# Optimization experiments

Measured on AMD Instinct MI355X. Metric: run time of the kernel, lower is better.

The kernel has to match this reference:

```python
import jax, jax.numpy as jnp
import numpy as np
import math

B, S, D, H = 16, 1024, 512, 8
DPH = D // H


def _lorentz_linear(x, W, b, log_scale):
    # LorentzLinear.forward: linear map then project onto hyperboloid
    x = x @ W.T + b
    time = jax.nn.sigmoid(x[..., :1]) * jnp.exp(log_scale) + 1.0 + 1e-4
    rest = x[..., 1:]
    sq = jnp.clip(jnp.sum(rest * rest, axis=-1, keepdims=True), 1e-8, None)
    scale = (time * time - 1.0) / sq
    return jnp.concatenate([time, rest * jnp.sqrt(scale)], axis=-1)


def setup_inputs() -> dict:
    key = jax.random.key(0)
    ks = jax.random.split(key, 16)
    stdv = 1.0 / math.sqrt(D)

    def mk_w(k):
        W = jax.random.uniform(k, (D, D), minval=-stdv, maxval=stdv, dtype=jnp.float32)
        return W.at[:, 0].set(0.0)  # reset_parameters zeroes column 0

    inp = {
        'key': jax.random.normal(ks[0], (B, S, D), dtype=jnp.float32),
        'value': jax.random.normal(ks[1], (B, S, D), dtype=jnp.float32),
        'query': jax.random.normal(ks[2], (B, S, D), dtype=jnp.float32),
        'Wq': mk_w(ks[3]), 'bq': jnp.zeros((D,), jnp.float32), 'lsq': jnp.asarray(math.log(10.0), jnp.float32),
        'Wk': mk_w(ks[4]), 'bk': jnp.zeros((D,), jnp.float32), 'lsk': jnp.asarray(math.log(10.0), jnp.float32),
        'Wv': mk_w(ks[5]), 'bv': jnp.zeros((D,), jnp.float32), 'lsv': jnp.asarray(math.log(10.0), jnp.float32),
        'attn_scale': jnp.asarray([math.sqrt(D)], jnp.float32),
        'attn_bias': jnp.zeros((), jnp.float32),
    }
    return inp


def reference(key, value, query, Wq, bq, lsq, Wk, bk, lsk, Wv, bv, lsv, attn_scale, attn_bias):
    q = _lorentz_linear(query, Wq, bq, lsq)  # [B,S,D]
    k = _lorentz_linear(key, Wk, bk, lsk)
    v = _lorentz_linear(value, Wv, bv, lsv)

    def shape(x):
        b, s, _ = x.shape
        return x.reshape(b, s, H, DPH).transpose(0, 2, 1, 3)  # [B,H,S,dph]

    q, k, v = shape(q), shape(k), shape(v)

    # Minkowski signature (-,+,...,+) on the per-head feature dim
    sgn = jnp.concatenate([-jnp.ones((1,), q.dtype), jnp.ones((DPH - 1,), q.dtype)])

    # attn = (2 + 2 * cinner(q, k)) / scale + bias  (no softmax, per source)
    attn = (2.0 + 2.0 * jnp.einsum('bhqd,bhkd->bhqk', q * sgn, k)) / attn_scale + attn_bias

    # mid_point: ave = attn @ v, then normalize by sqrt(|<ave,ave>_L|)
    ave = jnp.einsum('bhqk,bhkd->bhqd', attn, v)
    inner = jnp.sum(ave * ave * sgn, axis=-1, keepdims=True)  # Lorentz inner product
    denom = jnp.sqrt(jnp.clip(jnp.abs(inner), 1e-8, None))
    ctx = ave / denom  # [B,H,S,dph]

    b = ctx.shape[0]
    return ctx.transpose(0, 2, 1, 3).reshape(b, -1, H * DPH)  # [B,S,D]
```

## Files before the change

kernel.cpp:

```cpp
#include <hip/hip_runtime.h>
#include <stdint.h>

#define B_    16
#define S_    1024
#define D_    512
#define H_    8
#define DPH_  64
#define MTOT  (B_*S_)

typedef __attribute__((ext_vector_type(8))) short  short8;
typedef __attribute__((ext_vector_type(4))) float  float4v;
typedef __attribute__((ext_vector_type(4))) ushort u16x4;

__device__ inline float bf2f(ushort u) {
    union { uint32_t u; float f; } c; c.u = ((uint32_t)u) << 16; return c.f;
}
__device__ inline ushort f2bf(float f) {
    union { float f; uint32_t u; } c; c.f = f;
    uint32_t x = c.u;
    return (ushort)((x + 0x7fffu + ((x >> 16) & 1u)) >> 16);
}
__device__ inline bool mode_f32(const void* as) {
    return ((const ushort*)as)[0] == (ushort)0x04F3u;
}

typedef __attribute__((address_space(1))) uint32_t glob_u32;
typedef __attribute__((address_space(3))) uint32_t lds_u32;
__device__ __forceinline__ void gload16(const ushort* g, ushort* l) {
    __builtin_amdgcn_global_load_lds((glob_u32*)g, (lds_u32*)l, 16, 0, 0);
}

__global__ __launch_bounds__(256) void convert_w(
    const void* __restrict__ Wq, const void* __restrict__ Wk,
    const void* __restrict__ Wv, const void* __restrict__ as_flag,
    ushort* __restrict__ WP)
{
    if (!mode_f32(as_flag)) return;
    const int idx = blockIdx.x * 256 + threadIdx.x;
    const int z   = idx >> 16;
    const int off = idx & 65535;
    const float* W = z == 0 ? (const float*)Wq
                   : z == 1 ? (const float*)Wk : (const float*)Wv;
    const float4 v = ((const float4*)W)[off];
    ushort* whi = WP + (size_t)z * 524288;
    ushort* wlo = whi + 262144;
    u16x4 h, l;
    #pragma unroll
    for (int q = 0; q < 4; ++q) {
        const float f = (&v.x)[q];
        const ushort hi = f2bf(f);
        h[q] = hi;
        l[q] = f2bf(f - bf2f(hi));
    }
    *(u16x4*)&whi[off * 4] = h;
    *(u16x4*)&wlo[off * 4] = l;
}

__global__ __launch_bounds__(256) void gemm_proj(
    const void* __restrict__ Xq, const void* __restrict__ Xk, const void* __restrict__ Xv,
    const void* __restrict__ Wq, const void* __restrict__ Wk, const void* __restrict__ Wv,
    const void* __restrict__ bq, const void* __restrict__ bk, const void* __restrict__ bv,
    const void* __restrict__ as_flag, const ushort* __restrict__ Wplanes,
    float* __restrict__ Yq, float* __restrict__ Yk, float* __restrict__ Yv,
    float* __restrict__ RowY0, float* __restrict__ RowSq)
{
    const int z = blockIdx.z;
    const void* X    = z == 0 ? Xq : (z == 1 ? Xk : Xv);
    const void* W    = z == 0 ? Wq : (z == 1 ? Wk : Wv);
    const void* bias = z == 0 ? bq : (z == 1 ? bk : bv);
    float*      Y    = z == 0 ? Yq : (z == 1 ? Yk : Yv);
    const bool  f32  = mode_f32(as_flag);

    const int m0   = blockIdx.x * 128;
    const int n0   = blockIdx.y * 128;
    const int tid  = threadIdx.x;
    const int lane = tid & 63;
    const int w    = tid >> 6;
    const int wm   = w >> 1, wn = w & 1;

    __shared__ __align__(16) char smem[32768];
    ushort* s16 = (ushort*)smem;

    float4v acc[4][4];
    #pragma unroll
    for (int i = 0; i < 4; ++i)
        #pragma unroll
        for (int j = 0; j < 4; ++j)
            acc[i][j] = (float4v){0.f, 0.f, 0.f, 0.f};

    const int fr = lane & 15;
    const int fk = (lane >> 4) * 8;

    if (!f32) {
        int offA[4], offB[4];
        #pragma unroll
        for (int i = 0; i < 4; ++i) offA[i] = (wm * 64 + i * 16 + fr) * 32 + fk;
        #pragma unroll
        for (int j = 0; j < 4; ++j) offB[j] = (wn * 64 + j * 16 + fr) * 32 + fk;
        const ushort* Xu = (const ushort*)X;
        const ushort* Wu = (const ushort*)W;
        const int rsub = lane >> 2;
        const int cg   = (lane & 3) * 8;
        const ushort* gA0 = Xu + (size_t)(m0 + w * 16      + rsub) * D_ + cg;
        const ushort* gA1 = Xu + (size_t)(m0 + w * 16 + 64 + rsub) * D_ + cg;
        const ushort* gB0 = Wu + (size_t)(n0 + w * 16      + rsub) * D_ + cg;
        const ushort* gB1 = Wu + (size_t)(n0 + w * 16 + 64 + rsub) * D_ + cg;
        const int dA0 = w * 512;
        const int dA1 = 2048 + w * 512;

        gload16(gA0, &s16[dA0]);
        gload16(gA1, &s16[dA1]);
        gload16(gB0, &s16[4096 + dA0]);
        gload16(gB1, &s16[4096 + dA1]);
        __syncthreads();

        int cur = 0;
        for (int kt = 32; kt < D_; kt += 32) {
            const int nb = (cur ^ 1) * 8192;
            gload16(gA0 + kt, &s16[nb + dA0]);
            gload16(gA1 + kt, &s16[nb + dA1]);
            gload16(gB0 + kt, &s16[nb + 4096 + dA0]);
            gload16(gB1 + kt, &s16[nb + 4096 + dA1]);
            const ushort* bb = &s16[cur * 8192];
            short8 ah[4], bh[4];
            #pragma unroll
            for (int i = 0; i < 4; ++i) ah[i] = *(const short8*)&bb[offA[i]];
            #pragma unroll
            for (int j = 0; j < 4; ++j) bh[j] = *(const short8*)&bb[4096 + offB[j]];
            #pragma unroll
            for (int i = 0; i < 4; ++i)
                #pragma unroll
                for (int j = 0; j < 4; ++j)
                    acc[i][j] = __builtin_amdgcn_mfma_f32_16x16x32_bf16(ah[i], bh[j], acc[i][j], 0, 0, 0);
            __syncthreads();
            cur ^= 1;
        }
        {
            const ushort* bb = &s16[cur * 8192];
            short8 ah[4], bh[4];
            #pragma unroll
            for (int i = 0; i < 4; ++i) ah[i] = *(const short8*)&bb[offA[i]];
            #pragma unroll
            for (int j = 0; j < 4; ++j) bh[j] = *(const short8*)&bb[4096 + offB[j]];
            #pragma unroll
            for (int i = 0; i < 4; ++i)
                #pragma unroll
                for (int j = 0; j < 4; ++j)
                    acc[i][j] = __builtin_amdgcn_mfma_f32_16x16x32_bf16(ah[i], bh[j], acc[i][j], 0, 0, 0);
        }
    } else {
        const float*  Xf   = (const float*)X;
        const ushort* WhiZ = Wplanes + (size_t)z * 524288;
        const ushort* WloZ = WhiZ + 262144;

        int wrow[4], wc4[4], woff[4];
        #pragma unroll
        for (int it = 0; it < 4; ++it) {
            const int c = tid + it * 256;
            const int row = c >> 3, c4 = (c & 7) * 4;
            wrow[it] = row; wc4[it] = c4;
            woff[it] = row * 32 + ((((c4 >> 3) + (row >> 1)) & 3) << 3) + (c4 & 4);
        }
        const int rsub  = lane >> 2;
        const int sG    = lane & 3;
        const int rowB0 = w * 16 + rsub;
        const int rowB1 = 64 + w * 16 + rsub;
        const int g0 = ((sG - (rowB0 >> 1)) & 3) * 8;
        const int g1 = ((sG - (rowB1 >> 1)) & 3) * 8;
        const ushort* pBh0 = WhiZ + (size_t)(n0 + rowB0) * D_ + g0;
        const ushort* pBh1 = WhiZ + (size_t)(n0 + rowB1) * D_ + g1;
        const ushort* pBl0 = WloZ + (size_t)(n0 + rowB0) * D_ + g0;
        const ushort* pBl1 = WloZ + (size_t)(n0 + rowB1) * D_ + g1;
        ushort* dBh0 = &s16[8192  + w * 512];
        ushort* dBh1 = &s16[8192  + 2048 + w * 512];
        ushort* dBl0 = &s16[12288 + w * 512];
        ushort* dBl1 = &s16[12288 + 2048 + w * 512];

        int offAs[4], offBs[4];
        #pragma unroll
        for (int i = 0; i < 4; ++i) {
            const int row = wm * 64 + i * 16 + fr;
            offAs[i] = row * 32 + ((((fk >> 3) + (row >> 1)) & 3) << 3);
        }
        #pragma unroll
        for (int j = 0; j < 4; ++j) {
            const int row = wn * 64 + j * 16 + fr;
            offBs[j] = row * 32 + ((((fk >> 3) + (row >> 1)) & 3) << 3);
        }

        for (int kt = 0; kt < D_; kt += 32) {
            __syncthreads();
            gload16(pBh0 + kt, dBh0);
            gload16(pBh1 + kt, dBh1);
            gload16(pBl0 + kt, dBl0);
            gload16(pBl1 + kt, dBl1);
            #pragma unroll
            for (int it = 0; it < 4; ++it) {
                const float4 fa = *(const float4*)&Xf[(size_t)(m0 + wrow[it]) * D_ + kt + wc4[it]];
                u16x4 ah4, al4;
                #pragma unroll
                for (int q = 0; q < 4; ++q) {
                    const float fav = (&fa.x)[q];
                    union { float f; uint32_t u; } cc; cc.f = fav;
                    const ushort ha = (ushort)(cc.u >> 16);
                    ah4[q] = ha;
                    al4[q] = f2bf(fav - bf2f(ha));
                }
                *(u16x4*)&s16[woff[it]]        = ah4;
                *(u16x4*)&s16[4096 + woff[it]] = al4;
            }
            __syncthreads();
            short8 ah[4], al[4], bh[4], bl[4];
            #pragma unroll
            for (int i = 0; i < 4; ++i) {
                ah[i] = *(const short8*)&s16[offAs[i]];
                al[i] = *(const short8*)&s16[4096 + offAs[i]];
            }
            #pragma unroll
            for (int j = 0; j < 4; ++j) {
                bh[j] = *(const short8*)&s16[8192  + offBs[j]];
                bl[j] = *(const short8*)&s16[12288 + offBs[j]];
            }
            #pragma unroll
            for (int i = 0; i < 4; ++i)
                #pragma unroll
                for (int j = 0; j < 4; ++j) {
                    acc[i][j] = __builtin_amdgcn_mfma_f32_16x16x32_bf16(ah[i], bh[j], acc[i][j], 0, 0, 0);
                    acc[i][j] = __builtin_amdgcn_mfma_f32_16x16x32_bf16(al[i], bh[j], acc[i][j], 0, 0, 0);
                    acc[i][j] = __builtin_amdgcn_mfma_f32_16x16x32_bf16(ah[i], bl[j], acc[i][j], 0, 0, 0);
                }
        }
    }

    __syncthreads();
    float* sRS = (float*)smem;
    const int er = lane >> 4;
    float bvf[4];
    #pragma unroll
    for (int j = 0; j < 4; ++j) {
        const int n = n0 + wn * 64 + j * 16 + fr;
        bvf[j] = f32 ? ((const float*)bias)[n] : bf2f(((const ushort*)bias)[n]);
    }
    #pragma unroll
    for (int i = 0; i < 4; ++i)
        #pragma unroll
        for (int r = 0; r < 4; ++r) {
            const int row = wm * 64 + i * 16 + er * 4 + r;
            const int m = m0 + row;
            float rsum = 0.f;
            #pragma unroll
            for (int j = 0; j < 4; ++j) {
                const int n = n0 + wn * 64 + j * 16 + fr;
                const float y = acc[i][j][r] + bvf[j];
                Y[(size_t)m * D_ + n] = y;
                if (n != 0) rsum += y * y;
            }
            rsum += __shfl_xor(rsum, 1, 64);
            rsum += __shfl_xor(rsum, 2, 64);
            rsum += __shfl_xor(rsum, 4, 64);
            rsum += __shfl_xor(rsum, 8, 64);
            if (fr == 0) sRS[wn * 128 + row] = rsum;
            if (blockIdx.y == 0 && wn == 0 && fr == 0)
                RowY0[z * MTOT + m] = acc[i][0][r] + bvf[0];
        }
    __syncthreads();
    if (tid < 128) {
        const float v = sRS[tid] + sRS[128 + tid];
        atomicAdd(&RowSq[z * MTOT + m0 + tid], v);
    }
}

__global__ __launch_bounds__(256) void rowfix(
    float* __restrict__ T, float* __restrict__ A,
    const void* __restrict__ lq, const void* __restrict__ lk, const void* __restrict__ lv,
    const void* __restrict__ as_flag)
{
    const int idx = blockIdx.x * 256 + threadIdx.x;
    const int z = idx >> 14;
    const bool f32 = mode_f32(as_flag);
    const void* lsp = z == 0 ? lq : (z == 1 ? lk : lv);
    const float ls = f32 ? ((const float*)lsp)[0] : bf2f(((const ushort*)lsp)[0]);
    const float y0 = T[idx];
    const float sq = fmaxf(A[idx], 1e-8f);
    const float t = (1.f / (1.f + expf(-y0))) * expf(ls) + 1.0f + 1e-4f;
    T[idx] = t;
    A[idx] = sqrtf((t * t - 1.0f) / sq);
}

__global__ __launch_bounds__(256) void kv_k(
    const float* __restrict__ Yk, const float* __restrict__ Yv,
    const float* __restrict__ T, const float* __restrict__ A,
    float* __restrict__ KV, float* __restrict__ Vs)
{
    const int bh = blockIdx.x;
    const int sp = blockIdx.y;
    const int b = bh >> 3, h = bh & 7;
    const int t = threadIdx.x;
    const int td = t & 15, te = t >> 4;

    __shared__ float sK[16][64];
    __shared__ float sV[16][64];

    float acc[4][4] = {};
    float vs[4] = {0.f, 0.f, 0.f, 0.f};

    const int r  = t >> 4;
    const int c4 = (t & 15) * 4;
    const size_t mbase = (size_t)b * S_ + (size_t)sp * 128;

    for (int sc = 0; sc < 128; sc += 16) {
        const size_t m = mbase + sc + r;
        __syncthreads();
        float4 kr = *(const float4*)&Yk[m * D_ + h * DPH_ + c4];
        float4 vr = *(const float4*)&Yv[m * D_ + h * DPH_ + c4];
        const float ak = A[MTOT + m],     tk = T[MTOT + m];
        const float av = A[2 * MTOT + m], tv = T[2 * MTOT + m];
        kr.x *= ak; kr.y *= ak; kr.z *= ak; kr.w *= ak;
        vr.x *= av; vr.y *= av; vr.z *= av; vr.w *= av;
        if (h == 0 && c4 == 0) { kr.x = tk; vr.x = tv; }
        *(float4*)&sK[r][c4] = kr;
        *(float4*)&sV[r][c4] = vr;
        __syncthreads();
        #pragma unroll
        for (int rr = 0; rr < 16; ++rr) {
            const float4 k4 = *(const float4*)&sK[rr][te * 4];
            const float4 v4 = *(const float4*)&sV[rr][td * 4];
            #pragma unroll
            for (int i = 0; i < 4; ++i)
                #pragma unroll
                for (int j = 0; j < 4; ++j)
                    acc[i][j] += (&k4.x)[i] * (&v4.x)[j];
            #pragma unroll
            for (int j = 0; j < 4; ++j) vs[j] += (&v4.x)[j];
        }
    }

    #pragma unroll
    for (int i = 0; i < 4; ++i)
        #pragma unroll
        for (int j = 0; j < 4; ++j)
            atomicAdd(&KV[(size_t)bh * 4096 + (te * 4 + i) * 64 + td * 4 + j],
                      acc[i][j]);
    if (te == 0) {
        #pragma unroll
        for (int j = 0; j < 4; ++j)
            atomicAdd(&Vs[(size_t)bh * 64 + td * 4 + j], vs[j]);
    }
}

__global__ __launch_bounds__(256) void ave_norm(
    const float* __restrict__ Yq, const float* __restrict__ T, const float* __restrict__ A,
    const float* __restrict__ KV, const float* __restrict__ Vs,
    const void* __restrict__ as_ptr, const void* __restrict__ ab_ptr,
    void* __restrict__ outp)
{
    const int bh = blockIdx.x >> 3;
    const int st = blockIdx.x & 7;
    const int b = bh >> 3, h = bh & 7;
    const int s0 = st * 128;
    const int t = threadIdx.x;
    const int lane = t & 63;
    const int w = t >> 6;
    const bool f32 = mode_f32(as_ptr);

    __shared__ ushort sKVh[64 * 64];
    __shared__ ushort sKVl[64 * 64];
    __shared__ ushort sQh[128 * 64];
    __shared__ ushort sQl[128 * 64];
    __shared__ float  sVs[64];

    #pragma unroll
    for (int i = 0; i < 16; ++i) {
        const int idx = t + i * 256;
        const int e = idx >> 6, d = idx & 63;
        const float v = KV[(size_t)bh * 4096 + idx];
        const ushort hi = f2bf(v);
        sKVh[d * 64 + e] = hi;
        sKVl[d * 64 + e] = f2bf(v - bf2f(hi));
    }
    if (t < 64) sVs[t] = Vs[(size_t)bh * 64 + t];
    #pragma unroll
    for (int i = 0; i < 8; ++i) {
        const int idx = t + i * 256;
        const int row = idx >> 4, c4 = (idx & 15) * 4;
        const size_t m = (size_t)b * S_ + s0 + row;
        const float4 q4 = *(const float4*)&Yq[m * D_ + h * DPH_ + c4];
        const float alpha = A[m], tim = T[m];
        #pragma unroll
        for (int q = 0; q < 4; ++q) {
            const int col = c4 + q;
            float val = (&q4.x)[q] * alpha;
            if (h == 0 && col == 0) val = tim;
            if (col == 0) val = -val;
            const ushort hi = f2bf(val);
            sQh[row * 64 + col] = hi;
            sQl[row * 64 + col] = f2bf(val - bf2f(hi));
        }
    }
    __syncthreads();

    const float asv = f32 ? ((const float*)as_ptr)[0] : bf2f(((const ushort*)as_ptr)[0]);
    const float abv = f32 ? ((const float*)ab_ptr)[0] : bf2f(((const ushort*)ab_ptr)[0]);
    const float c1f = 2.0f / asv;
    const float c0f = c1f + abv;

    const int fr = lane & 15, fq = lane >> 4;

    float4v acc[2][4];
    #pragma unroll
    for (int mi = 0; mi < 2; ++mi)
        #pragma unroll
        for (int j = 0; j < 4; ++j)
            acc[mi][j] = (float4v){0.f, 0.f, 0.f, 0.f};

    #pragma unroll
    for (int kk = 0; kk < 2; ++kk) {
        const int ko = kk * 32 + fq * 8;
        short8 ah[2], al[2], bh4[4], bl4[4];
        #pragma unroll
        for (int mi = 0; mi < 2; ++mi) {
            ah[mi] = *(const short8*)&sQh[(w * 32 + mi * 16 + fr) * 64 + ko];
            al[mi] = *(const short8*)&sQl[(w * 32 + mi * 16 + fr) * 64 + ko];
        }
        #pragma unroll
        for (int j = 0; j < 4; ++j) {
            bh4[j] = *(const short8*)&sKVh[(j * 16 + fr) * 64 + ko];
            bl4[j] = *(const short8*)&sKVl[(j * 16 + fr) * 64 + ko];
        }
        #pragma unroll
        for (int mi = 0; mi < 2; ++mi)
            #pragma unroll
            for (int j = 0; j < 4; ++j) {
                acc[mi][j] = __builtin_amdgcn_mfma_f32_16x16x32_bf16(ah[mi], bh4[j], acc[mi][j], 0, 0, 0);
                acc[mi][j] = __builtin_amdgcn_mfma_f32_16x16x32_bf16(ah[mi], bl4[j], acc[mi][j], 0, 0, 0);
                acc[mi][j] = __builtin_amdgcn_mfma_f32_16x16x32_bf16(al[mi], bh4[j], acc[mi][j], 0, 0, 0);
            }
    }

    #pragma unroll
    for (int mi = 0; mi < 2; ++mi) {
        float avev[4][4];
        float part[4] = {0.f, 0.f, 0.f, 0.f};
        #pragma unroll
        for (int j = 0; j < 4; ++j) {
            const float vsn = sVs[j * 16 + fr];
            #pragma unroll
            for (int r = 0; r < 4; ++r) {
                const float a = c1f * acc[mi][j][r] + c0f * vsn;
                avev[j][r] = a;
                part[r] += (j == 0 && fr == 0) ? -(a * a) : (a * a);
            }
        }
        #pragma unroll
        for (int off = 1; off < 16; off <<= 1)
            #pragma unroll
            for (int r = 0; r < 4; ++r)
                part[r] += __shfl_xor(part[r], off, 64);
        float rd[4];
        #pragma unroll
        for (int r = 0; r < 4; ++r)
            rd[r] = 1.0f / sqrtf(fmaxf(fabsf(part[r]), 1e-8f));
        #pragma unroll
        for (int j = 0; j < 4; ++j)
            #pragma unroll
            for (int r = 0; r < 4; ++r) {
                const int srow = s0 + w * 32 + mi * 16 + fq * 4 + r;
                const size_t oidx = ((size_t)b * S_ + srow) * D_ + h * DPH_ + j * 16 + fr;
                const float cv = avev[j][r] * rd[r];
                if (f32) ((float*)outp)[oidx] = cv;
                else     ((ushort*)outp)[oidx] = f2bf(cv);
            }
    }
}

extern "C" void kernel_launch(void* const* d_in, const int* in_sizes, int n_in,
                              void* d_out, int out_size, void* d_ws, size_t ws_size,
                              hipStream_t stream)
{
    const void* key    = d_in[0];
    const void* value  = d_in[1];
    const void* query  = d_in[2];
    const void* Wq     = d_in[3];
    const void* bq     = d_in[4];
    const void* lsq    = d_in[5];
    const void* Wk     = d_in[6];
    const void* bk     = d_in[7];
    const void* lsk    = d_in[8];
    const void* Wv     = d_in[9];
    const void* bv     = d_in[10];
    const void* lsv    = d_in[11];
    const void* ascale = d_in[12];
    const void* abias  = d_in[13];

    char* ws = (char*)d_ws;
    float*  Yq    = (float*)(ws + 0);
    float*  Yk    = (float*)(ws + 33554432);
    float*  Yv    = (float*)(ws + 67108864);
    float*  T     = (float*)(ws + 100663296);
    float*  Alpha = (float*)(ws + 100859904);
    ushort* WPL   = (ushort*)(ws + 101056512);
    float*  KV    = (float*)(ws + 101056512);
    float*  Vs    = (float*)(ws + 103153664);

    hipMemsetAsync(ws + 100859904, 0, 196608, stream);

    convert_w<<<768, 256, 0, stream>>>(Wq, Wk, Wv, ascale, WPL);

    gemm_proj<<<dim3(MTOT / 128, D_ / 128, 3), 256, 0, stream>>>(
        query, key, value, Wq, Wk, Wv, bq, bk, bv, ascale, WPL,
        Yq, Yk, Yv, T, Alpha);

    hipMemsetAsync(ws + 101056512, 0, 2129920, stream);

    rowfix<<<(3 * MTOT) / 256, 256, 0, stream>>>(T, Alpha, lsq, lsk, lsv, ascale);
    kv_k<<<dim3(B_ * H_, 8), 256, 0, stream>>>(Yk, Yv, T, Alpha, KV, Vs);
    ave_norm<<<B_ * H_ * (S_ / 128), 256, 0, stream>>>(
        Yq, T, Alpha, KV, Vs, ascale, abias, d_out);
}
```

Measured before the change: 333.8 us.

## Fuse rowfix into consumers, swizzle LDS layout, merge memsets

Removes the separate rowfix kernel and recomputes the sigmoid time component and the row scale factor inline in kv_k and ave_norm from the raw row values. Adds an XOR swizzle to the shared-memory layout of Q and KV in ave_norm to avoid LDS bank conflicts, and writes Q as vectorized 4-element stores. Moves the converted-weight scratch buffer into the output buffer so the two memsets become one contiguous memset. In exchange, the per-row transcendental work is recomputed redundantly by every thread in the consumer kernels.

```diff
diff --git a/kernel.cpp b/kernel.cpp
--- a/kernel.cpp
+++ b/kernel.cpp
@@ -270,26 +270,11 @@
     }
 }
 
-__global__ __launch_bounds__(256) void rowfix(
-    float* __restrict__ T, float* __restrict__ A,
-    const void* __restrict__ lq, const void* __restrict__ lk, const void* __restrict__ lv,
-    const void* __restrict__ as_flag)
-{
-    const int idx = blockIdx.x * 256 + threadIdx.x;
-    const int z = idx >> 14;
-    const bool f32 = mode_f32(as_flag);
-    const void* lsp = z == 0 ? lq : (z == 1 ? lk : lv);
-    const float ls = f32 ? ((const float*)lsp)[0] : bf2f(((const ushort*)lsp)[0]);
-    const float y0 = T[idx];
-    const float sq = fmaxf(A[idx], 1e-8f);
-    const float t = (1.f / (1.f + expf(-y0))) * expf(ls) + 1.0f + 1e-4f;
-    T[idx] = t;
-    A[idx] = sqrtf((t * t - 1.0f) / sq);
-}
-
 __global__ __launch_bounds__(256) void kv_k(
     const float* __restrict__ Yk, const float* __restrict__ Yv,
     const float* __restrict__ T, const float* __restrict__ A,
+    const void* __restrict__ lk, const void* __restrict__ lv,
+    const void* __restrict__ as_flag,
     float* __restrict__ KV, float* __restrict__ Vs)
 {
     const int bh = blockIdx.x;
@@ -297,6 +282,9 @@
     const int b = bh >> 3, h = bh & 7;
     const int t = threadIdx.x;
     const int td = t & 15, te = t >> 4;
+    const bool f32 = mode_f32(as_flag);
+    const float elsk = expf(f32 ? ((const float*)lk)[0] : bf2f(((const ushort*)lk)[0]));
+    const float elsv = expf(f32 ? ((const float*)lv)[0] : bf2f(((const ushort*)lv)[0]));
 
     __shared__ float sK[16][64];
     __shared__ float sV[16][64];
@@ -313,8 +301,12 @@
         __syncthreads();
         float4 kr = *(const float4*)&Yk[m * D_ + h * DPH_ + c4];
         float4 vr = *(const float4*)&Yv[m * D_ + h * DPH_ + c4];
-        const float ak = A[MTOT + m],     tk = T[MTOT + m];
-        const float av = A[2 * MTOT + m], tv = T[2 * MTOT + m];
+        const float y0k = T[MTOT + m],     sqk = A[MTOT + m];
+        const float y0v = T[2 * MTOT + m], sqv = A[2 * MTOT + m];
+        const float tk = (1.f / (1.f + expf(-y0k))) * elsk + 1.0f + 1e-4f;
+        const float tv = (1.f / (1.f + expf(-y0v))) * elsv + 1.0f + 1e-4f;
+        const float ak = sqrtf((tk * tk - 1.0f) / fmaxf(sqk, 1e-8f));
+        const float av = sqrtf((tv * tv - 1.0f) / fmaxf(sqv, 1e-8f));
         kr.x *= ak; kr.y *= ak; kr.z *= ak; kr.w *= ak;
         vr.x *= av; vr.y *= av; vr.z *= av; vr.w *= av;
         if (h == 0 && c4 == 0) { kr.x = tk; vr.x = tv; }
@@ -351,6 +343,7 @@
 __global__ __launch_bounds__(256) void ave_norm(
     const float* __restrict__ Yq, const float* __restrict__ T, const float* __restrict__ A,
     const float* __restrict__ KV, const float* __restrict__ Vs,
+    const void* __restrict__ lq,
     const void* __restrict__ as_ptr, const void* __restrict__ ab_ptr,
     void* __restrict__ outp)
 {
@@ -362,6 +355,7 @@
     const int lane = t & 63;
     const int w = t >> 6;
     const bool f32 = mode_f32(as_ptr);
+    const float elsq = expf(f32 ? ((const float*)lq)[0] : bf2f(((const ushort*)lq)[0]));
 
     __shared__ ushort sKVh[64 * 64];
     __shared__ ushort sKVl[64 * 64];
@@ -375,8 +369,9 @@
         const int e = idx >> 6, d = idx & 63;
         const float v = KV[(size_t)bh * 4096 + idx];
         const ushort hi = f2bf(v);
-        sKVh[d * 64 + e] = hi;
-        sKVl[d * 64 + e] = f2bf(v - bf2f(hi));
+        const int off = d * 64 + (e ^ ((d & 7) << 3));
+        sKVh[off] = hi;
+        sKVl[off] = f2bf(v - bf2f(hi));
     }
     if (t < 64) sVs[t] = Vs[(size_t)bh * 64 + t];
     #pragma unroll
@@ -385,7 +380,10 @@
         const int row = idx >> 4, c4 = (idx & 15) * 4;
         const size_t m = (size_t)b * S_ + s0 + row;
         const float4 q4 = *(const float4*)&Yq[m * D_ + h * DPH_ + c4];
-        const float alpha = A[m], tim = T[m];
+        const float y0 = T[m], sq = A[m];
+        const float tim = (1.f / (1.f + expf(-y0))) * elsq + 1.0f + 1e-4f;
+        const float alpha = sqrtf((tim * tim - 1.0f) / fmaxf(sq, 1e-8f));
+        u16x4 qh, ql;
         #pragma unroll
         for (int q = 0; q < 4; ++q) {
             const int col = c4 + q;
@@ -393,9 +391,12 @@
             if (h == 0 && col == 0) val = tim;
             if (col == 0) val = -val;
             const ushort hi = f2bf(val);
-            sQh[row * 64 + col] = hi;
-            sQl[row * 64 + col] = f2bf(val - bf2f(hi));
-        }
+            qh[q] = hi;
+            ql[q] = f2bf(val - bf2f(hi));
+        }
+        const int c4s = ((((c4 >> 3) ^ (row & 7)) << 3) | (c4 & 4));
+        *(u16x4*)&sQh[row * 64 + c4s] = qh;
+        *(u16x4*)&sQl[row * 64 + c4s] = ql;
     }
     __syncthreads();
 
@@ -419,13 +420,17 @@
         short8 ah[2], al[2], bh4[4], bl4[4];
         #pragma unroll
         for (int mi = 0; mi < 2; ++mi) {
-            ah[mi] = *(const short8*)&sQh[(w * 32 + mi * 16 + fr) * 64 + ko];
-            al[mi] = *(const short8*)&sQl[(w * 32 + mi * 16 + fr) * 64 + ko];
+            const int rowA = w * 32 + mi * 16 + fr;
+            const int koA  = (((ko >> 3) ^ (rowA & 7)) << 3);
+            ah[mi] = *(const short8*)&sQh[rowA * 64 + koA];
+            al[mi] = *(const short8*)&sQl[rowA * 64 + koA];
         }
         #pragma unroll
         for (int j = 0; j < 4; ++j) {
-            bh4[j] = *(const short8*)&sKVh[(j * 16 + fr) * 64 + ko];
-            bl4[j] = *(const short8*)&sKVl[(j * 16 + fr) * 64 + ko];
+            const int rowB = j * 16 + fr;
+            const int koB  = (((ko >> 3) ^ (rowB & 7)) << 3);
+            bh4[j] = *(const short8*)&sKVh[rowB * 64 + koB];
+            bl4[j] = *(const short8*)&sKVl[rowB * 64 + koB];
         }
         #pragma unroll
         for (int mi = 0; mi < 2; ++mi)
@@ -498,11 +503,11 @@
     float*  Yv    = (float*)(ws + 67108864);
     float*  T     = (float*)(ws + 100663296);
     float*  Alpha = (float*)(ws + 100859904);
-    ushort* WPL   = (ushort*)(ws + 101056512);
     float*  KV    = (float*)(ws + 101056512);
     float*  Vs    = (float*)(ws + 103153664);
-
-    hipMemsetAsync(ws + 100859904, 0, 196608, stream);
+    ushort* WPL   = (ushort*)d_out;
+
+    hipMemsetAsync(ws + 100859904, 0, 2326528, stream);
 
     convert_w<<<768, 256, 0, stream>>>(Wq, Wk, Wv, ascale, WPL);
 
@@ -510,10 +515,9 @@
         query, key, value, Wq, Wk, Wv, bq, bk, bv, ascale, WPL,
         Yq, Yk, Yv, T, Alpha);
 
-    hipMemsetAsync(ws + 101056512, 0, 2129920, stream);
-
-    rowfix<<<(3 * MTOT) / 256, 256, 0, stream>>>(T, Alpha, lsq, lsk, lsv, ascale);
-    kv_k<<<dim3(B_ * H_, 8), 256, 0, stream>>>(Yk, Yv, T, Alpha, KV, Vs);
+    kv_k<<<dim3(B_ * H_, 8), 256, 0, stream>>>(
+        Yk, Yv, T, Alpha, lsk, lsv, ascale, KV, Vs);
+
     ave_norm<<<B_ * H_ * (S_ / 128), 256, 0, stream>>>(
-        Yq, T, Alpha, KV, Vs, ascale, abias, d_out);
-}
+        Yq, T, Alpha, KV, Vs, lsq, ascale, abias, d_out);
+}
```

Measured after the change: 322.8 us. -3.3%, faster.
